# Kernel optimization log

Measured on AMD Instinct MI355X. Metric: run time of the kernel, lower is better.

The kernel has to match this reference:

```python
import jax, jax.numpy as jnp
import numpy as np

EPS = float(np.finfo(np.float32).eps)  # matches torch.finfo(float32).eps
N_PTS, K_DIM, N_BINS = 1_000_000, 3, 21  # wv_tilde last dim = 2*N_BINS+1 = 43


def setup_inputs() -> dict:
    key = jax.random.key(0)
    k1, k2 = jax.random.split(key)
    # y in the open unit interval (points on the unit hypercube, per-coordinate)
    y = jax.random.uniform(k1, (N_PTS, K_DIM), jnp.float32, 1e-4, 1.0 - 1e-4)
    # network-predicted unnormalized widths/heights: [N, k, 2b+1]
    wv_tilde = jax.random.normal(k2, (N_PTS, K_DIM, 2 * N_BINS + 1), jnp.float32)
    return {"y": y, "wv_tilde": wv_tilde}


def _gather(t, idx):
    # gather along last axis with [..., 1] int index -> [...]
    return jnp.take_along_axis(t, idx, axis=-1)[..., 0]


def pwquad_flow(y, wv_tilde):
    """Faithful JAX port of ElementWisePWQuadraticTransform.flow (with jacobian)."""
    D = wv_tilde.shape[-1]
    nv = (D + 1) // 2                      # ceil(D/2) = b+1 vertex heights
    v_tilde = wv_tilde[..., :nv]           # [N,k,b+1]
    w_tilde = wv_tilde[..., nv:]           # [N,k,b]
    b = w_tilde.shape[-1]

    # normalized bin widths and their cumulative sums
    w = jnp.exp(w_tilde)
    wsum = jnp.cumsum(w, axis=-1)
    wnorm = wsum[..., -1:]
    w = w / wnorm
    wsum = wsum / wnorm
    zeros = jnp.zeros(wsum.shape[:-1] + (1,), wsum.dtype)
    wsum_shift = jnp.concatenate([zeros, wsum], axis=-1)   # [N,k,b+1]

    # modified softmax for vertex heights of the derivative (integrates to 1)
    ve = jnp.exp(v_tilde)
    trap = (ve[..., :-1] + ve[..., 1:]) * 0.5 * w          # trapezoid areas
    v = jnp.maximum(ve / trap.sum(-1, keepdims=True), 1e-6)  # [N,k,b+1]

    # cumulative CDF values at bin edges
    vw = jnp.concatenate(
        [zeros, jnp.cumsum((v[..., :-1] + v[..., 1:]) * 0.5 * w, axis=-1)],
        axis=-1)                                           # [N,k,b+1]

    # argmax-based bin search (identical to torch implementation)
    finder = jnp.where(vw > y[..., None], 0.0, 1.0)
    cat = jnp.concatenate([jnp.full_like(zeros, EPS), finder * (vw + 1.0)], axis=-1)
    mx = jnp.argmax(cat, axis=-1) - 1
    edges = jnp.clip(mx, 0, b - 1).astype(jnp.int32)[..., None]  # [N,k,1]

    v0 = _gather(v, edges)
    v1 = _gather(v, edges + 1)
    we = _gather(w, edges)

    # quadratic solve: (a/2) t^2 + bq t + c = 0  within the bin
    a = (v1 - v0) * we
    bq = v0 * we
    c = _gather(vw, edges) - y
    a = jnp.where(jnp.abs(a) < EPS, EPS, a)
    d = jnp.maximum(bq * bq - 2.0 * a * c, 0.0)
    sq = jnp.sqrt(d)
    sol1 = (-bq - sq) / a
    sol2 = (-bq + sq) / a
    sol = jnp.where((sol1 >= 0.0) & (sol1 < 1.0), sol1, sol2)
    sol = jnp.clip(sol, EPS, 1.0 - EPS)

    x = we * sol + _gather(wsum_shift, edges)
    x = jnp.clip(x, EPS, 1.0 - EPS)

    # log|det J| = -sum log(lerp(v0, v1, sol))
    logj = -jnp.sum(jnp.log(v0 + (v1 - v0) * sol), axis=-1, keepdims=True)
    return x, logj


def reference(y, wv_tilde):
    return pwquad_flow(y, wv_tilde)
```

## Files before the change

kernel.cpp:

```cpp
#include <hip/hip_runtime.h>
#include <math.h>

#define NROWS        3000000
#define NPTS         1000000
#define NTHREADS     64
#define ROWS_PER_BLK 192
#define NBINS        21
#define NV           22
#define DROW         43
#define F_PER_BLK    (ROWS_PER_BLK * DROW)
#define F4_PER_BLK   (F_PER_BLK / 4)
#define NBLOCKS      (NROWS / ROWS_PER_BLK)

#define AS1 __attribute__((address_space(1)))
#define AS3 __attribute__((address_space(3)))

__device__ __forceinline__ void gload16(const void* g, void* l) {
    __builtin_amdgcn_global_load_lds((const AS1 void*)g, (AS3 void*)l, 16, 0, 0);
}

__global__ __launch_bounds__(NTHREADS) void pwquad_kernel(
    const float* __restrict__ y,
    const float* __restrict__ wv,
    float* __restrict__ out)
{
    __shared__ float buf[F_PER_BLK];
    __shared__ float yb[ROWS_PER_BLK];

    const int tid = threadIdx.x;
    const int b   = blockIdx.x;
    const float EPSF = 1.1920929e-07f;

    {
        const float4* s = reinterpret_cast<const float4*>(wv) + (size_t)b * F4_PER_BLK;
        float4* d = reinterpret_cast<float4*>(buf);
#pragma unroll
        for (int it = 0; it < 32; ++it)
            gload16(s + it * NTHREADS + tid, d + it * NTHREADS + tid);
        if (tid < 16)
            gload16(s + 32 * NTHREADS + tid, d + 32 * NTHREADS + tid);
        if (tid < 48)
            gload16(reinterpret_cast<const float4*>(y) + (size_t)b * 48 + tid,
                    reinterpret_cast<float4*>(yb) + tid);
    }
    asm volatile("s_waitcnt vmcnt(0)" ::: "memory");

    float logj = 0.f;

    for (int r = 0; r < 3; ++r) {
        const int rrow = 3 * tid + r;
        const float* myrow = &buf[rrow * DROW];
        const float yv = yb[rrow];

        float w[NBINS];
        float wnorm = 0.f;
#pragma unroll
        for (int j = 0; j < NBINS; ++j) { w[j] = __expf(myrow[NV + j]); wnorm += w[j]; }
        const float invw = 1.0f / wnorm;
#pragma unroll
        for (int j = 0; j < NBINS; ++j) w[j] *= invw;

        float v[NV];
#pragma unroll
        for (int i = 0; i < NV; ++i) v[i] = __expf(myrow[i]);
        float T = 0.f;
#pragma unroll
        for (int j = 0; j < NBINS; ++j) T += (v[j] + v[j + 1]) * 0.5f * w[j];
        const float invT = 1.0f / T;
#pragma unroll
        for (int i = 0; i < NV; ++i) v[i] = fmaxf(v[i] * invT, 1e-6f);

        float vw = 0.f, wsum = 0.f;
        float vwe = 0.f, wse = 0.f;
        float v0 = v[0], v1 = v[1], we = w[0];
#pragma unroll
        for (int j = 0; j < 20; ++j) {
            const float inc = (v[j] + v[j + 1]) * 0.5f * w[j];
            vw += inc;
            wsum += w[j];
            const bool q = (vw <= yv);
            vwe = q ? vw       : vwe;
            wse = q ? wsum     : wse;
            v0  = q ? v[j + 1] : v0;
            v1  = q ? v[j + 2] : v1;
            we  = q ? w[j + 1] : we;
        }

        float a = (v1 - v0) * we;
        const float bq = v0 * we;
        const float cc = vwe - yv;
        a = (fabsf(a) < EPSF) ? EPSF : a;
        const float dd = fmaxf(bq * bq - 2.0f * a * cc, 0.f);
        const float sq = sqrtf(dd);
        const float sol1 = (-bq - sq) / a;
        const float sol2 = (-bq + sq) / a;
        float sol = (sol1 >= 0.f && sol1 < 1.f) ? sol1 : sol2;
        sol = fminf(fmaxf(sol, EPSF), 1.f - EPSF);
        float x = we * sol + wse;
        x = fminf(fmaxf(x, EPSF), 1.f - EPSF);

        out[(size_t)b * ROWS_PER_BLK + rrow] = x;
        logj += __logf(v0 + (v1 - v0) * sol);
    }

    out[NROWS + (size_t)b * NTHREADS + tid] = -logj;
}

extern "C" void kernel_launch(void* const* d_in, const int* in_sizes, int n_in,
                              void* d_out, int out_size, void* d_ws, size_t ws_size,
                              hipStream_t stream) {
    const float* y  = (const float*)d_in[0];
    const float* wv = (const float*)d_in[1];
    float* out = (float*)d_out;

    pwquad_kernel<<<NBLOCKS, NTHREADS, 0, stream>>>(y, wv, out);
}
```

Baseline: 122.0 us.

## Assign one row per thread with smaller blocks and shuffle-based logdet reduction

Blocks shrink from 192 to 60 rows so each thread handles one row instead of looping over three, and the per-point log-determinant is summed across three adjacent lanes with warp shuffles. This raises the number of blocks and cuts per-thread serial work, aiming for more parallelism and latency hiding; launch bounds now request higher occupancy. In exchange, 4 of 64 lanes sit idle, the LDS staging per block is smaller, and the loads of 60×43 floats are less aligned to the 16-byte chunking.

```diff
diff --git a/kernel.cpp b/kernel.cpp
--- a/kernel.cpp
+++ b/kernel.cpp
@@ -2,9 +2,8 @@
 #include <math.h>
 
 #define NROWS        3000000
-#define NPTS         1000000
 #define NTHREADS     64
-#define ROWS_PER_BLK 192
+#define ROWS_PER_BLK 60
 #define NBINS        21
 #define NV           22
 #define DROW         43
@@ -19,7 +18,7 @@
     __builtin_amdgcn_global_load_lds((const AS1 void*)g, (AS3 void*)l, 16, 0, 0);
 }
 
-__global__ __launch_bounds__(NTHREADS) void pwquad_kernel(
+__global__ __launch_bounds__(NTHREADS, 4) void pwquad_kernel(
     const float* __restrict__ y,
     const float* __restrict__ wv,
     float* __restrict__ out)
@@ -32,25 +31,23 @@
     const float EPSF = 1.1920929e-07f;
 
     {
-        const float4* s = reinterpret_cast<const float4*>(wv) + (size_t)b * F4_PER_BLK;
+        const float4* s = reinterpret_cast<const float4*>(wv + (size_t)b * F_PER_BLK);
         float4* d = reinterpret_cast<float4*>(buf);
 #pragma unroll
-        for (int it = 0; it < 32; ++it)
+        for (int it = 0; it < 10; ++it)
             gload16(s + it * NTHREADS + tid, d + it * NTHREADS + tid);
-        if (tid < 16)
-            gload16(s + 32 * NTHREADS + tid, d + 32 * NTHREADS + tid);
-        if (tid < 48)
-            gload16(reinterpret_cast<const float4*>(y) + (size_t)b * 48 + tid,
+        if (tid < (F4_PER_BLK - 10 * NTHREADS))
+            gload16(s + 10 * NTHREADS + tid, d + 10 * NTHREADS + tid);
+        if (tid < (ROWS_PER_BLK / 4))
+            gload16(reinterpret_cast<const float4*>(y + (size_t)b * ROWS_PER_BLK) + tid,
                     reinterpret_cast<float4*>(yb) + tid);
     }
     asm volatile("s_waitcnt vmcnt(0)" ::: "memory");
 
-    float logj = 0.f;
-
-    for (int r = 0; r < 3; ++r) {
-        const int rrow = 3 * tid + r;
-        const float* myrow = &buf[rrow * DROW];
-        const float yv = yb[rrow];
+    float ltv = 0.f;
+    if (tid < ROWS_PER_BLK) {
+        const float yv = yb[tid];
+        const float* myrow = &buf[tid * DROW];
 
         float w[NBINS];
         float wnorm = 0.f;
@@ -99,11 +96,15 @@
         float x = we * sol + wse;
         x = fminf(fmaxf(x, EPSF), 1.f - EPSF);
 
-        out[(size_t)b * ROWS_PER_BLK + rrow] = x;
-        logj += __logf(v0 + (v1 - v0) * sol);
+        out[(size_t)b * ROWS_PER_BLK + tid] = x;
+        ltv = __logf(v0 + (v1 - v0) * sol);
     }
 
-    out[NROWS + (size_t)b * NTHREADS + tid] = -logj;
+    const float t1 = __shfl(ltv, (tid + 1) & 63);
+    const float t2 = __shfl(ltv, (tid + 2) & 63);
+    if (tid < ROWS_PER_BLK && (tid % 3) == 0) {
+        out[NROWS + (size_t)b * (ROWS_PER_BLK / 3) + tid / 3] = -(ltv + t1 + t2);
+    }
 }
 
 extern "C" void kernel_launch(void* const* d_in, const int* in_sizes, int n_in,
```

After: 105.1 us. -13.9%, faster.

## Assign one row per thread and reduce log-det via wave shuffles

Applied to the files above, without the earlier changes.

Switches from 64 threads each handling 3 rows to 128-thread blocks where each lane handles a single row (60 rows per wave, 120 per block), and sums the per-point log-Jacobian across three adjacent lanes with shuffles. The direct global-to-LDS loads are replaced by register float4 loads followed by LDS stores and a __syncthreads. The aim is more parallelism and less serial per-thread work, at the cost of 4 idle lanes per wave, smaller blocks, and an extra register staging pass.

```diff
diff --git a/kernel.cpp b/kernel.cpp
--- a/kernel.cpp
+++ b/kernel.cpp
@@ -2,22 +2,15 @@
 #include <math.h>
 
 #define NROWS        3000000
-#define NPTS         1000000
-#define NTHREADS     64
-#define ROWS_PER_BLK 192
+#define NTHREADS     128
+#define ROWS_PER_BLK 120
+#define RPWAVE       60
 #define NBINS        21
 #define NV           22
 #define DROW         43
 #define F_PER_BLK    (ROWS_PER_BLK * DROW)
 #define F4_PER_BLK   (F_PER_BLK / 4)
 #define NBLOCKS      (NROWS / ROWS_PER_BLK)
-
-#define AS1 __attribute__((address_space(1)))
-#define AS3 __attribute__((address_space(3)))
-
-__device__ __forceinline__ void gload16(const void* g, void* l) {
-    __builtin_amdgcn_global_load_lds((const AS1 void*)g, (AS3 void*)l, 16, 0, 0);
-}
 
 __global__ __launch_bounds__(NTHREADS) void pwquad_kernel(
     const float* __restrict__ y,
@@ -34,23 +27,27 @@
     {
         const float4* s = reinterpret_cast<const float4*>(wv) + (size_t)b * F4_PER_BLK;
         float4* d = reinterpret_cast<float4*>(buf);
+        float4 r[10], rt, ry;
 #pragma unroll
-        for (int it = 0; it < 32; ++it)
-            gload16(s + it * NTHREADS + tid, d + it * NTHREADS + tid);
-        if (tid < 16)
-            gload16(s + 32 * NTHREADS + tid, d + 32 * NTHREADS + tid);
-        if (tid < 48)
-            gload16(reinterpret_cast<const float4*>(y) + (size_t)b * 48 + tid,
-                    reinterpret_cast<float4*>(yb) + tid);
+        for (int it = 0; it < 10; ++it) r[it] = s[it * NTHREADS + tid];
+        const bool tail = (tid < (F4_PER_BLK - 10 * NTHREADS));
+        if (tail) rt = s[10 * NTHREADS + tid];
+        const bool yl = (tid < (ROWS_PER_BLK / 4));
+        if (yl) ry = reinterpret_cast<const float4*>(y)[(size_t)b * (ROWS_PER_BLK / 4) + tid];
+#pragma unroll
+        for (int it = 0; it < 10; ++it) d[it * NTHREADS + tid] = r[it];
+        if (tail) d[10 * NTHREADS + tid] = rt;
+        if (yl) reinterpret_cast<float4*>(yb)[tid] = ry;
     }
-    asm volatile("s_waitcnt vmcnt(0)" ::: "memory");
+    __syncthreads();
 
-    float logj = 0.f;
+    const int wave = tid >> 6, lane = tid & 63;
+    const int rrow = wave * RPWAVE + lane;
+    float ltv = 0.f;
 
-    for (int r = 0; r < 3; ++r) {
-        const int rrow = 3 * tid + r;
+    if (lane < RPWAVE) {
+        const float yv = yb[rrow];
         const float* myrow = &buf[rrow * DROW];
-        const float yv = yb[rrow];
 
         float w[NBINS];
         float wnorm = 0.f;
@@ -100,10 +97,14 @@
         x = fminf(fmaxf(x, EPSF), 1.f - EPSF);
 
         out[(size_t)b * ROWS_PER_BLK + rrow] = x;
-        logj += __logf(v0 + (v1 - v0) * sol);
+        ltv = __logf(v0 + (v1 - v0) * sol);
     }
 
-    out[NROWS + (size_t)b * NTHREADS + tid] = -logj;
+    const float t1 = __shfl(ltv, (lane + 1) & 63);
+    const float t2 = __shfl(ltv, (lane + 2) & 63);
+    if (lane < RPWAVE && (lane % 3) == 0) {
+        out[NROWS + (size_t)b * (ROWS_PER_BLK / 3) + (rrow / 3)] = -(ltv + t1 + t2);
+    }
 }
 
 extern "C" void kernel_launch(void* const* d_in, const int* in_sizes, int n_in,
```

After: 103.7 us. -15.0%, faster.
